# Kernel optimization log

Hardware: AMD Instinct MI355X
Metric: run time of the kernel (lower is better)

## Reference

```python
import jax, jax.numpy as jnp
import numpy as np

N_NODES = 100_000
N_EDGES = 800_000
D = 96
BN_EPS = 1e-5
LEAKY_SLOPE = 0.01


def setup_inputs() -> dict:
    key = jax.random.key(0)
    ks = jax.random.split(key, 9)
    x = jax.random.normal(ks[0], (N_NODES, D), dtype=jnp.float32)
    edge_index = jax.random.randint(ks[1], (2, N_EDGES), 0, N_NODES, dtype=jnp.int64)
    s = 0.05
    return {
        "x": x,
        "edge_index": edge_index,
        # SAGEConv #1 (mean aggregator, bias=False)
        "W_self1": jax.random.normal(ks[2], (D, D), dtype=jnp.float32) * s,
        "W_neigh1": jax.random.normal(ks[3], (D, D), dtype=jnp.float32) * s,
        # SAGEConv #2 (pool aggregator): fc_pool has bias, fc_self/fc_neigh bias=False
        "W_pool": jax.random.normal(ks[4], (D, D), dtype=jnp.float32) * s,
        "b_pool": jax.random.normal(ks[5], (D,), dtype=jnp.float32) * s,
        "W_self2": jax.random.normal(ks[6], (D, D), dtype=jnp.float32) * s,
        "W_neigh2": jax.random.normal(ks[7], (D, D), dtype=jnp.float32) * s,
        # BatchNorm affine params
        "g1": jnp.ones((D,), jnp.float32),
        "beta1": jnp.zeros((D,), jnp.float32),
        "g2": jnp.ones((D,), jnp.float32),
        "beta2": jnp.zeros((D,), jnp.float32),
    }


def _batch_norm(h, gamma, beta):
    # training-mode BatchNorm1d: biased batch stats over nodes
    mu = h.mean(axis=0)
    var = jnp.mean(jnp.square(h - mu), axis=0)
    return gamma * (h - mu) * jax.lax.rsqrt(var + BN_EPS) + beta


def _forward(x, edge_index, W_self1, W_neigh1, W_pool, b_pool, W_self2, W_neigh2,
             g1, beta1, g2, beta2):
    src, dst = edge_index[0], edge_index[1]
    n = x.shape[0]
    deg = jax.ops.segment_sum(jnp.ones((src.shape[0],), x.dtype), dst, num_segments=n)

    # ---- SAGEConv (mean): h_neigh = mean_{u in N(v)} x_u ; out = x W_self + h_neigh W_neigh
    agg_sum = jax.ops.segment_sum(x[src], dst, num_segments=n)          # [N, D]
    h_mean = agg_sum / jnp.maximum(deg, 1.0)[:, None]                   # 0 for isolated nodes
    out1 = x @ W_self1 + h_mean @ W_neigh1
    out1 = _batch_norm(out1, g1, beta1)

    # ---- SAGEConv (pool): h_neigh = max_{u in N(v)} relu(x_u W_pool + b_pool)
    hp = jax.nn.relu(x @ W_pool + b_pool)                               # [N, D]
    agg_max = jax.ops.segment_max(hp[src], dst, num_segments=n)        # -inf where empty
    h_max = jnp.where(deg[:, None] > 0, agg_max, 0.0)
    out2 = x @ W_self2 + h_max @ W_neigh2
    out2 = _batch_norm(out2, g2, beta2)

    return jax.nn.leaky_relu(out1 + out2, negative_slope=LEAKY_SLOPE)


def reference(x, edge_index, W_self1, W_neigh1, W_pool, b_pool, W_self2, W_neigh2,
              g1, beta1, g2, beta2):
    return _forward(x, edge_index, W_self1, W_neigh1, W_pool, b_pool,
                    W_self2, W_neigh2, g1, beta1, g2, beta2)
```

## Files before the change

### kernel.cpp

```cpp
#include <hip/hip_runtime.h>

#define NN 100000
#define NE 800000
#define DD 96
#define NROWPAD 100096
#define GBLK 782
#define DBLK 391
#define SCAN_BLOCKS 100
#define SCAN_CHUNK 1000

typedef __attribute__((ext_vector_type(8))) short bf16x8;
typedef __attribute__((ext_vector_type(8))) unsigned short u16x8;
typedef __attribute__((ext_vector_type(4))) float f32x4;
typedef unsigned short u16;
typedef unsigned int u32;

#define MFMA16 __builtin_amdgcn_mfma_f32_16x16x32_bf16

#define OFF_DEG      0u
#define OFF_ROWSTART 100000u
#define OFF_CURSOR   200004u
#define OFF_BSUM     300004u
#define OFF_STATS    300132u
#define OFF_PARAMS   300516u
#define OFF_WT       300900u
#define OFF_CSR      323940u
#define OFF_XH       1123940u
#define OFF_HMBF     10733156u
#define OFF_HXBF     15537764u

__device__ __forceinline__ u16 f2b(float f) {
  u32 u = __float_as_uint(f);
  u += 0x7FFFu + ((u >> 16) & 1u);
  return (u16)(u >> 16);
}
__device__ __forceinline__ float b2f(short h) {
  return __uint_as_float(((u32)(u16)h) << 16);
}

__global__ void wprep_kernel(const float* __restrict__ Ws1, const float* __restrict__ Wn1,
                             const float* __restrict__ Ws2, const float* __restrict__ Wn2,
                             const float* __restrict__ Wp, u16* __restrict__ wt) {
  int idx = blockIdx.x * 256 + threadIdx.x;
  if (idx >= 5 * 9216) return;
  int m = idx / 9216, r = idx % 9216;
  int k = r / 96, c = r % 96;
  const float* W = (m == 0) ? Ws1 : (m == 1) ? Wn1 : (m == 2) ? Ws2 : (m == 3) ? Wn2 : Wp;
  wt[m * 9216 + c * 96 + k] = f2b(W[k * 96 + c]);
}

__global__ void deg_kernel(const int* __restrict__ dst, int* __restrict__ deg) {
  int e = blockIdx.x * blockDim.x + threadIdx.x;
  if (e >= NE) return;
  atomicAdd(&deg[dst[e]], 1);
}

__global__ void scan_sum_kernel(const int* __restrict__ deg, int* __restrict__ bsum) {
  __shared__ int red[256];
  int t = threadIdx.x;
  int base = blockIdx.x * SCAN_CHUNK;
  int s = 0;
  for (int i = t; i < SCAN_CHUNK; i += 256) s += deg[base + i];
  red[t] = s;
  __syncthreads();
  for (int off = 128; off > 0; off >>= 1) {
    if (t < off) red[t] += red[t + off];
    __syncthreads();
  }
  if (t == 0) bsum[blockIdx.x] = red[0];
}

__global__ void scan_bsum_kernel(int* __restrict__ bsum, int* __restrict__ row_start) {
  __shared__ int sm[128];
  int t = threadIdx.x;
  int v = (t < SCAN_BLOCKS) ? bsum[t] : 0;
  sm[t] = v;
  __syncthreads();
  for (int off = 1; off < 128; off <<= 1) {
    int u = 0;
    if (t >= off) u = sm[t - off];
    __syncthreads();
    if (t >= off) sm[t] += u;
    __syncthreads();
  }
  if (t < SCAN_BLOCKS) bsum[t] = sm[t] - v;
  if (t == SCAN_BLOCKS - 1) row_start[NN] = sm[t];
}

__global__ void scan_final_kernel(const int* __restrict__ deg,
                                  const int* __restrict__ bsum,
                                  int* __restrict__ row_start,
                                  int* __restrict__ cursor) {
  __shared__ int sm[256];
  int t = threadIdx.x;
  int base = blockIdx.x * SCAN_CHUNK + t * 4;
  int4 d = {0, 0, 0, 0};
  if (t < 250) d = *reinterpret_cast<const int4*>(deg + base);
  int tot = d.x + d.y + d.z + d.w;
  sm[t] = tot;
  __syncthreads();
  for (int off = 1; off < 256; off <<= 1) {
    int u = 0;
    if (t >= off) u = sm[t - off];
    __syncthreads();
    if (t >= off) sm[t] += u;
    __syncthreads();
  }
  if (t < 250) {
    int run = bsum[blockIdx.x] + sm[t] - tot;
    int4 rs;
    rs.x = run;
    rs.y = run + d.x;
    rs.z = run + d.x + d.y;
    rs.w = run + d.x + d.y + d.z;
    *reinterpret_cast<int4*>(row_start + base) = rs;
    *reinterpret_cast<int4*>(cursor + base) = rs;
  }
}

__global__ void fill_csr_kernel(const int* __restrict__ src,
                                const int* __restrict__ dst,
                                int* __restrict__ cursor,
                                int* __restrict__ csr) {
  int e = blockIdx.x * blockDim.x + threadIdx.x;
  if (e >= NE) return;
  int pos = atomicAdd(&cursor[dst[e]], 1);
  csr[pos] = src[e];
}

__global__ __launch_bounds__(512) void hp_gemm_kernel(const float* __restrict__ x,
                                                      const u16* __restrict__ wt,
                                                      const float* __restrict__ bp,
                                                      u16* __restrict__ xh) {
  __shared__ bf16x8 wl[1152];
  int t = threadIdx.x;
  const bf16x8* wg = reinterpret_cast<const bf16x8*>(wt + 4 * 9216);
  for (int j = t; j < 1152; j += 512) wl[j] = wg[j];
  __syncthreads();
  int w = t >> 6, lane = t & 63;
  int i = lane & 15, g = lane >> 4;
  int row_base = blockIdx.x * 128 + w * 16;
  int grow_a = row_base + i;
  int lrow = grow_a < NN ? grow_a : NN - 1;
  const float4* xr = reinterpret_cast<const float4*>(x + (size_t)lrow * 96);
  bf16x8* xhv = reinterpret_cast<bf16x8*>(xh);
  bf16x8 ax[3];
#pragma unroll
  for (int kb = 0; kb < 3; ++kb) {
    float4 p = xr[(kb * 4 + g) * 2];
    float4 q = xr[(kb * 4 + g) * 2 + 1];
    bf16x8 v;
    v[0] = (short)f2b(p.x); v[1] = (short)f2b(p.y); v[2] = (short)f2b(p.z); v[3] = (short)f2b(p.w);
    v[4] = (short)f2b(q.x); v[5] = (short)f2b(q.y); v[6] = (short)f2b(q.z); v[7] = (short)f2b(q.w);
    ax[kb] = v;
    xhv[(size_t)grow_a * 24 + kb * 4 + g] = v;
  }
  for (int nt = 0; nt < 6; ++nt) {
    f32x4 acc = {0.f, 0.f, 0.f, 0.f};
    int bch = (nt * 16 + i) * 12;
#pragma unroll
    for (int kb = 0; kb < 3; ++kb)
      acc = MFMA16(ax[kb], wl[bch + kb * 4 + g], acc, 0, 0, 0);
    int col = nt * 16 + i;
    float bias = bp[col];
#pragma unroll
    for (int r = 0; r < 4; ++r) {
      int grow = row_base + g * 4 + r;
      xh[(size_t)grow * 192 + 96 + col] = f2b(fmaxf(acc[r] + bias, 0.0f));
    }
  }
}

__global__ __launch_bounds__(256) void gather_kernel(const u16* __restrict__ xh,
                                                     const int* __restrict__ row_start,
                                                     const int* __restrict__ csr,
                                                     u16* __restrict__ hmbf,
                                                     u16* __restrict__ hxbf) {
  int t = threadIdx.x;
  int node = blockIdx.x * 32 + (t & 31);
  int slot = t >> 5;
  bool isMax = slot >= 4;
  if (node >= NN) return;
  int beg = row_start[node], end = row_start[node + 1];
  int cbase = slot * 3;
  const u16x8* XH = reinterpret_cast<const u16x8*>(xh);
  float s0[8], s1[8], s2[8];
  u16x8 m0, m1, m2;
#pragma unroll
  for (int j = 0; j < 8; ++j) {
    s0[j] = 0.f; s1[j] = 0.f; s2[j] = 0.f;
    m0[j] = 0; m1[j] = 0; m2[j] = 0;
  }
  int e = beg;
  int i0 = csr[(e < end) ? e : 0];
  int i1 = csr[(e + 1 < end) ? e + 1 : ((end > beg) ? end - 1 : 0)];
  for (; e + 2 <= end; e += 2) {
    int p2 = e + 2, p3 = e + 3;
    int n0 = csr[(p2 < end) ? p2 : end - 1];
    int n1 = csr[(p3 < end) ? p3 : end - 1];
    size_t b0 = (size_t)i0 * 24 + cbase;
    size_t b1 = (size_t)i1 * 24 + cbase;
    u16x8 u0 = XH[b0], u1 = XH[b0 + 1], u2 = XH[b0 + 2];
    u16x8 v0 = XH[b1], v1 = XH[b1 + 1], v2 = XH[b1 + 2];
    if (isMax) {
#pragma unroll
      for (int j = 0; j < 8; ++j) {
        u16 a = u0[j] > v0[j] ? u0[j] : v0[j]; m0[j] = m0[j] > a ? m0[j] : a;
        u16 b = u1[j] > v1[j] ? u1[j] : v1[j]; m1[j] = m1[j] > b ? m1[j] : b;
        u16 c = u2[j] > v2[j] ? u2[j] : v2[j]; m2[j] = m2[j] > c ? m2[j] : c;
      }
    } else {
#pragma unroll
      for (int j = 0; j < 8; ++j) {
        s0[j] += b2f((short)u0[j]) + b2f((short)v0[j]);
        s1[j] += b2f((short)u1[j]) + b2f((short)v1[j]);
        s2[j] += b2f((short)u2[j]) + b2f((short)v2[j]);
      }
    }
    i0 = n0; i1 = n1;
  }
  if (e < end) {
    size_t b0 = (size_t)i0 * 24 + cbase;
    u16x8 u0 = XH[b0], u1 = XH[b0 + 1], u2 = XH[b0 + 2];
    if (isMax) {
#pragma unroll
      for (int j = 0; j < 8; ++j) {
        m0[j] = m0[j] > u0[j] ? m0[j] : u0[j];
        m1[j] = m1[j] > u1[j] ? m1[j] : u1[j];
        m2[j] = m2[j] > u2[j] ? m2[j] : u2[j];
      }
    } else {
#pragma unroll
      for (int j = 0; j < 8; ++j) {
        s0[j] += b2f((short)u0[j]);
        s1[j] += b2f((short)u1[j]);
        s2[j] += b2f((short)u2[j]);
      }
    }
  }
  if (isMax) {
    u16x8* dv = reinterpret_cast<u16x8*>(hxbf);
    size_t ob = (size_t)node * 12 + (slot - 4) * 3;
    dv[ob] = m0; dv[ob + 1] = m1; dv[ob + 2] = m2;
  } else {
    float scl = (end > beg) ? 1.0f / (float)(end - beg) : 0.0f;
    u16x8 w0, w1, w2;
#pragma unroll
    for (int j = 0; j < 8; ++j) {
      w0[j] = f2b(s0[j] * scl);
      w1[j] = f2b(s1[j] * scl);
      w2[j] = f2b(s2[j] * scl);
    }
    u16x8* dv = reinterpret_cast<u16x8*>(hmbf);
    size_t ob = (size_t)node * 12 + slot * 3;
    dv[ob] = w0; dv[ob + 1] = w1; dv[ob + 2] = w2;
  }
}

__global__ __launch_bounds__(1024) void dualgemm_kernel(const u16* __restrict__ xh,
                                                        u16* __restrict__ hmbf,
                                                        u16* __restrict__ hxbf,
                                                        const u16* __restrict__ wt,
                                                        float* __restrict__ stats) {
  __shared__ bf16x8 wl[4608];
  __shared__ float smst[384];
  int t = threadIdx.x;
  const bf16x8* wg = reinterpret_cast<const bf16x8*>(wt);
  for (int j = t; j < 4608; j += 1024) wl[j] = wg[j];
  for (int j = t; j < 384; j += 1024) smst[j] = 0.f;
  __syncthreads();
  int w = t >> 6, lane = t & 63;
  int i = lane & 15, g = lane >> 4;
  int row_base = blockIdx.x * 256 + w * 16;
  size_t arowx = (size_t)(row_base + i) * 24;
  size_t arowh = (size_t)(row_base + i) * 12;
  bf16x8 ax[3], am[3], ah[3];
#pragma unroll
  for (int kb = 0; kb < 3; ++kb) {
    ax[kb] = reinterpret_cast<const bf16x8*>(xh)[arowx + kb * 4 + g];
    am[kb] = reinterpret_cast<const bf16x8*>(hmbf)[arowh + kb * 4 + g];
    ah[kb] = reinterpret_cast<const bf16x8*>(hxbf)[arowh + kb * 4 + g];
  }
  __syncthreads();
  for (int nt = 0; nt < 6; ++nt) {
    f32x4 a1 = {0.f, 0.f, 0.f, 0.f}, a2 = {0.f, 0.f, 0.f, 0.f};
    int bch = (nt * 16 + i) * 12;
#pragma unroll
    for (int kb = 0; kb < 3; ++kb) {
      int bc = bch + kb * 4 + g;
      a1 = MFMA16(ax[kb], wl[bc], a1, 0, 0, 0);
      a1 = MFMA16(am[kb], wl[1152 + bc], a1, 0, 0, 0);
      a2 = MFMA16(ax[kb], wl[2304 + bc], a2, 0, 0, 0);
      a2 = MFMA16(ah[kb], wl[3456 + bc], a2, 0, 0, 0);
    }
    int col = nt * 16 + i;
    float s1 = 0, q1 = 0, s2 = 0, q2 = 0;
#pragma unroll
    for (int r = 0; r < 4; ++r) {
      int grow = row_base + g * 4 + r;
      if (grow < NN) {
        float v = a1[r], u = a2[r];
        s1 += v; q1 += v * v; s2 += u; q2 += u * u;
        hmbf[(size_t)grow * 96 + col] = f2b(v);
        hxbf[(size_t)grow * 96 + col] = f2b(u);
      }
    }
    s1 += __shfl_xor(s1, 16); q1 += __shfl_xor(q1, 16);
    s2 += __shfl_xor(s2, 16); q2 += __shfl_xor(q2, 16);
    s1 += __shfl_xor(s1, 32); q1 += __shfl_xor(q1, 32);
    s2 += __shfl_xor(s2, 32); q2 += __shfl_xor(q2, 32);
    if (g == 0) {
      atomicAdd(&smst[col], s1);
      atomicAdd(&smst[96 + col], q1);
      atomicAdd(&smst[192 + col], s2);
      atomicAdd(&smst[288 + col], q2);
    }
  }
  __syncthreads();
  for (int j = t; j < 384; j += 1024) atomicAdd(&stats[j], smst[j]);
}

__global__ void finalize_kernel(const float* __restrict__ stats,
                                const float* __restrict__ g1, const float* __restrict__ beta1,
                                const float* __restrict__ g2, const float* __restrict__ beta2,
                                float* __restrict__ params) {
  int c = threadIdx.x;
  if (c >= 96) return;
  const float inv_n = 1.0f / NN;
  float mu1 = stats[c] * inv_n;
  float var1 = fmaxf(stats[96 + c] * inv_n - mu1 * mu1, 0.0f);
  float is1 = rsqrtf(var1 + 1e-5f);
  float a1 = g1[c] * is1;
  params[c] = a1;
  params[96 + c] = beta1[c] - a1 * mu1;
  float mu2 = stats[192 + c] * inv_n;
  float var2 = fmaxf(stats[288 + c] * inv_n - mu2 * mu2, 0.0f);
  float is2 = rsqrtf(var2 + 1e-5f);
  float a2 = g2[c] * is2;
  params[192 + c] = a2;
  params[288 + c] = beta2[c] - a2 * mu2;
}

__global__ __launch_bounds__(256) void final_kernel(const u16* __restrict__ o1,
                                                    const u16* __restrict__ o2,
                                                    const float* __restrict__ params,
                                                    float* __restrict__ out) {
  int idx = blockIdx.x * 256 + threadIdx.x;
  if (idx >= NN * 12) return;
  int c8 = idx % 12;
  bf16x8 v1 = reinterpret_cast<const bf16x8*>(o1)[idx];
  bf16x8 v2 = reinterpret_cast<const bf16x8*>(o2)[idx];
  const float4* P = reinterpret_cast<const float4*>(params);
  float4 A1l = P[c8 * 2],      A1h = P[c8 * 2 + 1];
  float4 B1l = P[24 + c8 * 2], B1h = P[24 + c8 * 2 + 1];
  float4 A2l = P[48 + c8 * 2], A2h = P[48 + c8 * 2 + 1];
  float4 B2l = P[72 + c8 * 2], B2h = P[72 + c8 * 2 + 1];
  float A1[8] = {A1l.x, A1l.y, A1l.z, A1l.w, A1h.x, A1h.y, A1h.z, A1h.w};
  float B1[8] = {B1l.x, B1l.y, B1l.z, B1l.w, B1h.x, B1h.y, B1h.z, B1h.w};
  float A2[8] = {A2l.x, A2l.y, A2l.z, A2l.w, A2h.x, A2h.y, A2h.z, A2h.w};
  float B2[8] = {B2l.x, B2l.y, B2l.z, B2l.w, B2h.x, B2h.y, B2h.z, B2h.w};
  float o[8];
#pragma unroll
  for (int j = 0; j < 8; ++j) {
    float v = A1[j] * b2f(v1[j]) + B1[j] + A2[j] * b2f(v2[j]) + B2[j];
    o[j] = v > 0.f ? v : 0.01f * v;
  }
  float4* ov = reinterpret_cast<float4*>(out);
  float4 lo = {o[0], o[1], o[2], o[3]}, hi = {o[4], o[5], o[6], o[7]};
  ov[idx * 2] = lo;
  ov[idx * 2 + 1] = hi;
}

extern "C" void kernel_launch(void* const* d_in, const int* in_sizes, int n_in,
                              void* d_out, int out_size, void* d_ws, size_t ws_size,
                              hipStream_t stream) {
  const float* x       = (const float*)d_in[0];
  const int*   ei      = (const int*)d_in[1];
  const float* W_self1 = (const float*)d_in[2];
  const float* W_neigh1= (const float*)d_in[3];
  const float* W_pool  = (const float*)d_in[4];
  const float* b_pool  = (const float*)d_in[5];
  const float* W_self2 = (const float*)d_in[6];
  const float* W_neigh2= (const float*)d_in[7];
  const float* g1      = (const float*)d_in[8];
  const float* beta1   = (const float*)d_in[9];
  const float* g2      = (const float*)d_in[10];
  const float* beta2   = (const float*)d_in[11];
  float* out = (float*)d_out;

  float* ws = (float*)d_ws;
  int*   deg       = (int*)(ws + OFF_DEG);
  int*   row_start = (int*)(ws + OFF_ROWSTART);
  int*   cursor    = (int*)(ws + OFF_CURSOR);
  int*   bsum      = (int*)(ws + OFF_BSUM);
  float* stats     = ws + OFF_STATS;
  float* params    = ws + OFF_PARAMS;
  u16*   wt        = (u16*)(ws + OFF_WT);
  int*   csr       = (int*)(ws + OFF_CSR);
  u16*   xh        = (u16*)(ws + OFF_XH);
  u16*   hmbf      = (u16*)(ws + OFF_HMBF);
  u16*   hxbf      = (u16*)(ws + OFF_HXBF);

  const int* src = ei;
  const int* dst = ei + NE;

  hipMemsetAsync(deg, 0, NN * sizeof(int), stream);
  hipMemsetAsync(stats, 0, 384 * sizeof(float), stream);

  wprep_kernel<<<(5 * 9216 + 255) / 256, 256, 0, stream>>>(W_self1, W_neigh1, W_self2,
                                                           W_neigh2, W_pool, wt);

  deg_kernel<<<(NE + 255) / 256, 256, 0, stream>>>(dst, deg);
  scan_sum_kernel<<<SCAN_BLOCKS, 256, 0, stream>>>(deg, bsum);
  scan_bsum_kernel<<<1, 128, 0, stream>>>(bsum, row_start);
  scan_final_kernel<<<SCAN_BLOCKS, 256, 0, stream>>>(deg, bsum, row_start, cursor);
  fill_csr_kernel<<<(NE + 255) / 256, 256, 0, stream>>>(src, dst, cursor, csr);

  hp_gemm_kernel<<<GBLK, 512, 0, stream>>>(x, wt, b_pool, xh);

  gather_kernel<<<(NN + 31) / 32, 256, 0, stream>>>(xh, row_start, csr, hmbf, hxbf);

  dualgemm_kernel<<<DBLK, 1024, 0, stream>>>(xh, hmbf, hxbf, wt, stats);
  finalize_kernel<<<1, 128, 0, stream>>>(stats, g1, beta1, g2, beta2, params);
  final_kernel<<<(NN * 12 + 255) / 256, 256, 0, stream>>>(hmbf, hxbf, params, out);
}
```

Baseline: 261.0 us.

## Recompute dual GEMM in output kernel instead of storing intermediates

The single GEMM kernel that wrote bf16 GEMM outputs back into the aggregation buffers is split in two. The first kernel now computes the GEMM only to accumulate BatchNorm statistics and writes nothing per element. A second kernel recomputes the same GEMM and applies BN, the add and leaky-ReLU directly into the output. This removes the intermediate bf16 writes and their re-read, and drops the old __syncthreads, at the cost of doing the MFMA work twice. It also avoids rounding the pre-BN values to bf16 before normalisation. Blocks shrink to 512 threads with an occupancy hint of 4 blocks.

```diff
diff --git a/kernel.cpp b/kernel.cpp
--- a/kernel.cpp
+++ b/kernel.cpp
@@ -5,7 +5,6 @@
 #define DD 96
 #define NROWPAD 100096
 #define GBLK 782
-#define DBLK 391
 #define SCAN_BLOCKS 100
 #define SCAN_CHUNK 1000
 
@@ -257,42 +256,48 @@
   }
 }
 
-__global__ __launch_bounds__(1024) void dualgemm_kernel(const u16* __restrict__ xh,
-                                                        u16* __restrict__ hmbf,
-                                                        u16* __restrict__ hxbf,
-                                                        const u16* __restrict__ wt,
-                                                        float* __restrict__ stats) {
+__global__ __launch_bounds__(512, 4) void stats_gemm_kernel(const u16* __restrict__ xh,
+                                                            const u16* __restrict__ hmbf,
+                                                            const u16* __restrict__ hxbf,
+                                                            const u16* __restrict__ wt,
+                                                            float* __restrict__ stats) {
   __shared__ bf16x8 wl[4608];
   __shared__ float smst[384];
   int t = threadIdx.x;
   const bf16x8* wg = reinterpret_cast<const bf16x8*>(wt);
-  for (int j = t; j < 4608; j += 1024) wl[j] = wg[j];
-  for (int j = t; j < 384; j += 1024) smst[j] = 0.f;
+  for (int j = t; j < 4608; j += 512) wl[j] = wg[j];
+  for (int j = t; j < 384; j += 512) smst[j] = 0.f;
   __syncthreads();
   int w = t >> 6, lane = t & 63;
   int i = lane & 15, g = lane >> 4;
-  int row_base = blockIdx.x * 256 + w * 16;
+  int row_base = blockIdx.x * 128 + w * 16;
   size_t arowx = (size_t)(row_base + i) * 24;
   size_t arowh = (size_t)(row_base + i) * 12;
-  bf16x8 ax[3], am[3], ah[3];
-#pragma unroll
-  for (int kb = 0; kb < 3; ++kb) {
-    ax[kb] = reinterpret_cast<const bf16x8*>(xh)[arowx + kb * 4 + g];
-    am[kb] = reinterpret_cast<const bf16x8*>(hmbf)[arowh + kb * 4 + g];
-    ah[kb] = reinterpret_cast<const bf16x8*>(hxbf)[arowh + kb * 4 + g];
-  }
-  __syncthreads();
+  bf16x8 ax0, ax1, ax2, am0, am1, am2, ah0, ah1, ah2;
+  {
+    const bf16x8* X = reinterpret_cast<const bf16x8*>(xh);
+    const bf16x8* M = reinterpret_cast<const bf16x8*>(hmbf);
+    const bf16x8* H = reinterpret_cast<const bf16x8*>(hxbf);
+    ax0 = X[arowx + g]; ax1 = X[arowx + 4 + g]; ax2 = X[arowx + 8 + g];
+    am0 = M[arowh + g]; am1 = M[arowh + 4 + g]; am2 = M[arowh + 8 + g];
+    ah0 = H[arowh + g]; ah1 = H[arowh + 4 + g]; ah2 = H[arowh + 8 + g];
+  }
+#pragma unroll
   for (int nt = 0; nt < 6; ++nt) {
     f32x4 a1 = {0.f, 0.f, 0.f, 0.f}, a2 = {0.f, 0.f, 0.f, 0.f};
-    int bch = (nt * 16 + i) * 12;
-#pragma unroll
-    for (int kb = 0; kb < 3; ++kb) {
-      int bc = bch + kb * 4 + g;
-      a1 = MFMA16(ax[kb], wl[bc], a1, 0, 0, 0);
-      a1 = MFMA16(am[kb], wl[1152 + bc], a1, 0, 0, 0);
-      a2 = MFMA16(ax[kb], wl[2304 + bc], a2, 0, 0, 0);
-      a2 = MFMA16(ah[kb], wl[3456 + bc], a2, 0, 0, 0);
-    }
+    int bch = (nt * 16 + i) * 12 + g;
+    a1 = MFMA16(ax0, wl[bch], a1, 0, 0, 0);
+    a1 = MFMA16(ax1, wl[bch + 4], a1, 0, 0, 0);
+    a1 = MFMA16(ax2, wl[bch + 8], a1, 0, 0, 0);
+    a1 = MFMA16(am0, wl[1152 + bch], a1, 0, 0, 0);
+    a1 = MFMA16(am1, wl[1152 + bch + 4], a1, 0, 0, 0);
+    a1 = MFMA16(am2, wl[1152 + bch + 8], a1, 0, 0, 0);
+    a2 = MFMA16(ax0, wl[2304 + bch], a2, 0, 0, 0);
+    a2 = MFMA16(ax1, wl[2304 + bch + 4], a2, 0, 0, 0);
+    a2 = MFMA16(ax2, wl[2304 + bch + 8], a2, 0, 0, 0);
+    a2 = MFMA16(ah0, wl[3456 + bch], a2, 0, 0, 0);
+    a2 = MFMA16(ah1, wl[3456 + bch + 4], a2, 0, 0, 0);
+    a2 = MFMA16(ah2, wl[3456 + bch + 8], a2, 0, 0, 0);
     int col = nt * 16 + i;
     float s1 = 0, q1 = 0, s2 = 0, q2 = 0;
 #pragma unroll
@@ -301,8 +306,6 @@
       if (grow < NN) {
         float v = a1[r], u = a2[r];
         s1 += v; q1 += v * v; s2 += u; q2 += u * u;
-        hmbf[(size_t)grow * 96 + col] = f2b(v);
-        hxbf[(size_t)grow * 96 + col] = f2b(u);
       }
     }
     s1 += __shfl_xor(s1, 16); q1 += __shfl_xor(q1, 16);
@@ -317,7 +320,7 @@
     }
   }
   __syncthreads();
-  for (int j = t; j < 384; j += 1024) atomicAdd(&stats[j], smst[j]);
+  for (int j = t; j < 384; j += 512) atomicAdd(&stats[j], smst[j]);
 }
 
 __global__ void finalize_kernel(const float* __restrict__ stats,
@@ -341,34 +344,62 @@
   params[288 + c] = beta2[c] - a2 * mu2;
 }
 
-__global__ __launch_bounds__(256) void final_kernel(const u16* __restrict__ o1,
-                                                    const u16* __restrict__ o2,
-                                                    const float* __restrict__ params,
-                                                    float* __restrict__ out) {
-  int idx = blockIdx.x * 256 + threadIdx.x;
-  if (idx >= NN * 12) return;
-  int c8 = idx % 12;
-  bf16x8 v1 = reinterpret_cast<const bf16x8*>(o1)[idx];
-  bf16x8 v2 = reinterpret_cast<const bf16x8*>(o2)[idx];
-  const float4* P = reinterpret_cast<const float4*>(params);
-  float4 A1l = P[c8 * 2],      A1h = P[c8 * 2 + 1];
-  float4 B1l = P[24 + c8 * 2], B1h = P[24 + c8 * 2 + 1];
-  float4 A2l = P[48 + c8 * 2], A2h = P[48 + c8 * 2 + 1];
-  float4 B2l = P[72 + c8 * 2], B2h = P[72 + c8 * 2 + 1];
-  float A1[8] = {A1l.x, A1l.y, A1l.z, A1l.w, A1h.x, A1h.y, A1h.z, A1h.w};
-  float B1[8] = {B1l.x, B1l.y, B1l.z, B1l.w, B1h.x, B1h.y, B1h.z, B1h.w};
-  float A2[8] = {A2l.x, A2l.y, A2l.z, A2l.w, A2h.x, A2h.y, A2h.z, A2h.w};
-  float B2[8] = {B2l.x, B2l.y, B2l.z, B2l.w, B2h.x, B2h.y, B2h.z, B2h.w};
-  float o[8];
-#pragma unroll
-  for (int j = 0; j < 8; ++j) {
-    float v = A1[j] * b2f(v1[j]) + B1[j] + A2[j] * b2f(v2[j]) + B2[j];
-    o[j] = v > 0.f ? v : 0.01f * v;
-  }
-  float4* ov = reinterpret_cast<float4*>(out);
-  float4 lo = {o[0], o[1], o[2], o[3]}, hi = {o[4], o[5], o[6], o[7]};
-  ov[idx * 2] = lo;
-  ov[idx * 2 + 1] = hi;
+__global__ __launch_bounds__(512, 4) void out_gemm_kernel(const u16* __restrict__ xh,
+                                                          const u16* __restrict__ hmbf,
+                                                          const u16* __restrict__ hxbf,
+                                                          const u16* __restrict__ wt,
+                                                          const float* __restrict__ params,
+                                                          float* __restrict__ out) {
+  __shared__ bf16x8 wl[4608];
+  __shared__ float pl[384];
+  int t = threadIdx.x;
+  const bf16x8* wg = reinterpret_cast<const bf16x8*>(wt);
+  for (int j = t; j < 4608; j += 512) wl[j] = wg[j];
+  for (int j = t; j < 384; j += 512) pl[j] = params[j];
+  __syncthreads();
+  int w = t >> 6, lane = t & 63;
+  int i = lane & 15, g = lane >> 4;
+  int row_base = blockIdx.x * 128 + w * 16;
+  size_t arowx = (size_t)(row_base + i) * 24;
+  size_t arowh = (size_t)(row_base + i) * 12;
+  bf16x8 ax0, ax1, ax2, am0, am1, am2, ah0, ah1, ah2;
+  {
+    const bf16x8* X = reinterpret_cast<const bf16x8*>(xh);
+    const bf16x8* M = reinterpret_cast<const bf16x8*>(hmbf);
+    const bf16x8* H = reinterpret_cast<const bf16x8*>(hxbf);
+    ax0 = X[arowx + g]; ax1 = X[arowx + 4 + g]; ax2 = X[arowx + 8 + g];
+    am0 = M[arowh + g]; am1 = M[arowh + 4 + g]; am2 = M[arowh + 8 + g];
+    ah0 = H[arowh + g]; ah1 = H[arowh + 4 + g]; ah2 = H[arowh + 8 + g];
+  }
+#pragma unroll
+  for (int nt = 0; nt < 6; ++nt) {
+    f32x4 a1 = {0.f, 0.f, 0.f, 0.f}, a2 = {0.f, 0.f, 0.f, 0.f};
+    int bch = (nt * 16 + i) * 12 + g;
+    a1 = MFMA16(ax0, wl[bch], a1, 0, 0, 0);
+    a1 = MFMA16(ax1, wl[bch + 4], a1, 0, 0, 0);
+    a1 = MFMA16(ax2, wl[bch + 8], a1, 0, 0, 0);
+    a1 = MFMA16(am0, wl[1152 + bch], a1, 0, 0, 0);
+    a1 = MFMA16(am1, wl[1152 + bch + 4], a1, 0, 0, 0);
+    a1 = MFMA16(am2, wl[1152 + bch + 8], a1, 0, 0, 0);
+    a2 = MFMA16(ax0, wl[2304 + bch], a2, 0, 0, 0);
+    a2 = MFMA16(ax1, wl[2304 + bch + 4], a2, 0, 0, 0);
+    a2 = MFMA16(ax2, wl[2304 + bch + 8], a2, 0, 0, 0);
+    a2 = MFMA16(ah0, wl[3456 + bch], a2, 0, 0, 0);
+    a2 = MFMA16(ah1, wl[3456 + bch + 4], a2, 0, 0, 0);
+    a2 = MFMA16(ah2, wl[3456 + bch + 8], a2, 0, 0, 0);
+    int col = nt * 16 + i;
+    float p1 = pl[col], c1 = pl[96 + col];
+    float p2 = pl[192 + col], c2 = pl[288 + col];
+#pragma unroll
+    for (int r = 0; r < 4; ++r) {
+      int grow = row_base + g * 4 + r;
+      if (grow < NN) {
+        float v = p1 * a1[r] + c1 + p2 * a2[r] + c2;
+        v = v > 0.f ? v : 0.01f * v;
+        out[(size_t)grow * 96 + col] = v;
+      }
+    }
+  }
 }
 
 extern "C" void kernel_launch(void* const* d_in, const int* in_sizes, int n_in,
@@ -420,7 +451,7 @@
 
   gather_kernel<<<(NN + 31) / 32, 256, 0, stream>>>(xh, row_start, csr, hmbf, hxbf);
 
-  dualgemm_kernel<<<DBLK, 1024, 0, stream>>>(xh, hmbf, hxbf, wt, stats);
+  stats_gemm_kernel<<<GBLK, 512, 0, stream>>>(xh, hmbf, hxbf, wt, stats);
   finalize_kernel<<<1, 128, 0, stream>>>(stats, g1, beta1, g2, beta2, params);
-  final_kernel<<<(NN * 12 + 255) / 256, 256, 0, stream>>>(hmbf, hxbf, params, out);
-}
+  out_gemm_kernel<<<GBLK, 512, 0, stream>>>(xh, hmbf, hxbf, wt, params, out);
+}
```

New measurement: 268.9 us. 1.03x slower.
